# Kernel tuning notes

Measured on AMD Instinct MI355X. Metric: run time of the kernel, lower is better.

## Reference

```python
import jax, jax.numpy as jnp
import numpy as np

N = 8192
D_IN = 512
D_OUT = 64
ALPHA = 0.2  # LeakyReLU negative slope
MASK_VAL = -9e15


def setup_inputs() -> dict:
    key = jax.random.key(0)
    k1, k2, k3, k4 = jax.random.split(key, 4)
    inp = jax.random.normal(k1, (N, D_IN), dtype=jnp.float32)
    adj = (jax.random.uniform(k2, (N, N)) < 0.05).astype(jnp.float32)
    adj = adj.at[jnp.arange(N), jnp.arange(N)].set(1.0)
    W = jax.random.normal(k3, (D_IN, D_OUT), dtype=jnp.float32) * 0.05
    a = jax.random.normal(k4, (2 * D_OUT, 1), dtype=jnp.float32) * 0.05
    return {"input": inp, "adj": adj, "W": W, "a": a}


def reference(input, adj, W, a):
    # h = input @ W : [n, out]
    h = input @ W
    # Algebraic equivalent of the dense pairwise concat:
    # e_ij = leakyrelu([h_i || h_j] . a) = leakyrelu(h_i.a1 + h_j.a2)
    a1, a2 = a[:D_OUT, 0], a[D_OUT:, 0]          # [out], [out]
    e = jax.nn.leaky_relu(
        (h @ a1)[:, None] + (h @ a2)[None, :],    # [n, n]
        negative_slope=ALPHA,
    )
    attention = jnp.where(adj > 0, e, MASK_VAL)
    attention = jax.nn.softmax(attention, axis=1)
    out = attention @ h                            # [n, out]
    return jax.nn.elu(out)                         # end=False branch
```

## Files before the change

### kernel.cpp

```cpp
#include <hip/hip_runtime.h>
#include <hip/hip_bf16.h>

#define N 8192
#define D_IN 512
#define D_OUT 64
#define ALPHA 0.2f
#define BM 16
#define BK 128
#define NSTEP (N / BK)

typedef __attribute__((ext_vector_type(4))) float f32x4;
typedef __attribute__((ext_vector_type(8))) short bf16x8;

static __device__ __forceinline__ unsigned pk_bf16(float lo, float hi) {
    unsigned ulo = __bfloat16_as_ushort(__float2bfloat16(lo));
    unsigned uhi = __bfloat16_as_ushort(__float2bfloat16(hi));
    return (uhi << 16) | ulo;
}

#define BARRIER() do { \
    asm volatile("s_waitcnt lgkmcnt(0)" ::: "memory"); \
    __builtin_amdgcn_sched_barrier(0); \
    __builtin_amdgcn_s_barrier(); \
    __builtin_amdgcn_sched_barrier(0); \
} while (0)

__global__ __launch_bounds__(256) void gat_h_kernel(
    const float* __restrict__ input, const float* __restrict__ W,
    const float* __restrict__ a, unsigned short* __restrict__ hbT,
    float* __restrict__ s1, float* __restrict__ s2)
{
    int wave = (blockIdx.x * 256 + threadIdx.x) >> 6;
    int lane = threadIdx.x & 63;
    int row0 = wave * 8;
    const float* in0 = input + (size_t)row0 * D_IN;
    float a1 = a[lane], a2 = a[D_OUT + lane];
    float acc[8];
#pragma unroll
    for (int r = 0; r < 8; ++r) acc[r] = 0.f;
#pragma unroll 4
    for (int k = 0; k < D_IN; ++k) {
        float wk = W[k * D_OUT + lane];
#pragma unroll
        for (int r = 0; r < 8; ++r)
            acc[r] = fmaf(in0[(size_t)r * D_IN + k], wk, acc[r]);
    }
    uint4 hv;
    hv.x = pk_bf16(acc[0], acc[1]);
    hv.y = pk_bf16(acc[2], acc[3]);
    hv.z = pk_bf16(acc[4], acc[5]);
    hv.w = pk_bf16(acc[6], acc[7]);
    *(uint4*)(hbT + (size_t)lane * N + row0) = hv;
#pragma unroll
    for (int r = 0; r < 8; ++r) {
        float p1 = acc[r] * a1;
        float p2 = acc[r] * a2;
#pragma unroll
        for (int off = 32; off; off >>= 1) {
            p1 += __shfl_xor(p1, off, 64);
            p2 += __shfl_xor(p2, off, 64);
        }
        if (lane == 0) { s1[row0 + r] = p1; s2[row0 + r] = p2; }
    }
}

struct Pref { float4 a0, a1; uint4 h0, h1, h2, h3; };

static __device__ __forceinline__ void issue(Pref& p, const float* ab,
                                             const unsigned short* hb, int j0) {
    p.a0 = *(const float4*)(ab + j0);
    p.a1 = *(const float4*)(ab + j0 + 4);
    p.h0 = *(const uint4*)(hb + j0);
    p.h1 = *(const uint4*)(hb + j0 + 8);
    p.h2 = *(const uint4*)(hb + j0 + 16);
    p.h3 = *(const uint4*)(hb + j0 + 24);
}

__global__ __launch_bounds__(256, 2) void gat_flash_kernel(
    const float* __restrict__ adj, const unsigned short* __restrict__ hbT,
    const float* __restrict__ s1, const float* __restrict__ s2,
    float* __restrict__ out)
{
    __shared__ float s2l[N];
    __shared__ __align__(16) unsigned char Pl[2][BM * BK * 2];
    __shared__ __align__(16) unsigned char Hl[2][D_OUT * BK * 2];
    __shared__ float lsl[BM];

    const int tid  = threadIdx.x;
    const int lane = tid & 63;
    const int wv   = tid >> 6;
    const int r    = tid >> 4;
    const int s    = tid & 15;
    const int hd   = tid >> 2;
    const int hc   = tid & 3;
    const int rg   = blockIdx.x * BM + r;

    {
        const float4* src = (const float4*)s2;
        float4* dst = (float4*)s2l;
        for (int i = tid; i < N / 4; i += 256) dst[i] = src[i];
    }
    const float* adj_base = adj + (size_t)rg * N + s * 8;
    const unsigned short* hb_base = hbT + (size_t)hd * N + hc * 32;
    float s1r = s1[rg];
    float eref;
    float lsum = 0.f;
    f32x4 acc = {0.f, 0.f, 0.f, 0.f};

    auto stage = [&](const Pref& p, int j0, int b) {
        float4 s2a = *(const float4*)(s2l + j0 + s * 8);
        float4 s2b = *(const float4*)(s2l + j0 + s * 8 + 4);
        const float* av0 = (const float*)&p.a0;
        const float* av1 = (const float*)&p.a1;
        const float* sv0 = (const float*)&s2a;
        const float* sv1 = (const float*)&s2b;
        float w[8];
#pragma unroll
        for (int z = 0; z < 4; ++z) {
            float e0 = s1r + sv0[z]; e0 = e0 > 0.f ? e0 : ALPHA * e0;
            float e1 = s1r + sv1[z]; e1 = e1 > 0.f ? e1 : ALPHA * e1;
            float w0 = __expf(e0 - eref);
            float w1 = __expf(e1 - eref);
            w[z]     = av0[z] > 0.f ? w0 : 0.f;
            w[z + 4] = av1[z] > 0.f ? w1 : 0.f;
        }
#pragma unroll
        for (int z = 0; z < 8; ++z) lsum += w[z];
        uint4 pk;
        pk.x = pk_bf16(w[0], w[1]); pk.y = pk_bf16(w[2], w[3]);
        pk.z = pk_bf16(w[4], w[5]); pk.w = pk_bf16(w[6], w[7]);
        *(uint4*)(&Pl[b][r * 256 + ((s * 16) ^ ((r & 7) << 4))]) = pk;
        *(uint4*)(&Hl[b][hd * 256 + ((hc * 64 +  0) ^ ((hd & 7) << 4))]) = p.h0;
        *(uint4*)(&Hl[b][hd * 256 + ((hc * 64 + 16) ^ ((hd & 7) << 4))]) = p.h1;
        *(uint4*)(&Hl[b][hd * 256 + ((hc * 64 + 32) ^ ((hd & 7) << 4))]) = p.h2;
        *(uint4*)(&Hl[b][hd * 256 + ((hc * 64 + 48) ^ ((hd & 7) << 4))]) = p.h3;
    };

    auto mfma_step = [&](int c) {
        const unsigned char* Pc = Pl[c];
        const unsigned char* Hc = Hl[c];
        const int i  = lane & 15;
        const int kb = lane >> 4;
        const int dd = wv * 16 + (lane & 15);
#pragma unroll
        for (int kk = 0; kk < 4; ++kk) {
            uint4 ua = *(const uint4*)(Pc + i * 256 + ((kk * 64 + kb * 16) ^ ((i & 7) << 4)));
            uint4 ub = *(const uint4*)(Hc + dd * 256 + ((kk * 64 + kb * 16) ^ ((dd & 7) << 4)));
            acc = __builtin_amdgcn_mfma_f32_16x16x32_bf16(
                __builtin_bit_cast(bf16x8, ua), __builtin_bit_cast(bf16x8, ub), acc, 0, 0, 0);
        }
    };

    Pref RA, RB;
    issue(RA, adj_base, hb_base, 0);
    issue(RB, adj_base, hb_base, BK);
    __syncthreads();
    {
        float ed = s1r + s2l[rg];
        eref = ed > 0.f ? ed : ALPHA * ed;
    }
    stage(RA, 0, 0);
    issue(RA, adj_base, hb_base, 2 * BK);
    BARRIER();

    for (int ks = 0; ks < NSTEP; ks += 2) {
        mfma_step(0);
        stage(RB, (ks + 1) * BK, 1);
        if (ks + 3 < NSTEP) issue(RB, adj_base, hb_base, (ks + 3) * BK);
        BARRIER();
        mfma_step(1);
        if (ks + 2 < NSTEP) {
            stage(RA, (ks + 2) * BK, 0);
            if (ks + 4 < NSTEP) issue(RA, adj_base, hb_base, (ks + 4) * BK);
        }
        BARRIER();
    }

#pragma unroll
    for (int off = 8; off; off >>= 1) lsum += __shfl_xor(lsum, off, 64);
    if ((tid & 15) == 0) lsl[r] = lsum;
    __syncthreads();

    const int dd = wv * 16 + (lane & 15);
#pragma unroll
    for (int reg = 0; reg < 4; ++reg) {
        int i = (lane >> 4) * 4 + reg;
        float o = acc[reg] / lsl[i];
        o = o > 0.f ? o : expm1f(o);
        out[(size_t)(blockIdx.x * BM + i) * 64 + dd] = o;
    }
}

extern "C" void kernel_launch(void* const* d_in, const int* in_sizes, int n_in,
                              void* d_out, int out_size, void* d_ws, size_t ws_size,
                              hipStream_t stream) {
    const float* input = (const float*)d_in[0];
    const float* adj   = (const float*)d_in[1];
    const float* W     = (const float*)d_in[2];
    const float* a     = (const float*)d_in[3];
    float* out = (float*)d_out;

    unsigned short* hbT = (unsigned short*)d_ws;
    float* s1 = (float*)(hbT + (size_t)N * D_OUT);
    float* s2 = s1 + N;

    gat_h_kernel<<<256, 256, 0, stream>>>(input, W, a, hbT, s1, s2);
    gat_flash_kernel<<<N / BM, 256, 0, stream>>>(adj, hbT, s1, s2, out);
}
```

Measured before the change: 123.5 us.

## Drop LDS s2 staging, prefetch s2 from global, raise occupancy

The flash kernel no longer copies the whole 32 KB s2 vector into shared memory at block start. Each thread now prefetches its s2 slice from global memory (L2-resident) together with adj and h, which frees LDS so three blocks can fit per CU instead of two. The projection kernel also gives each wave 4 rows instead of 8 and doubles the grid, for more parallelism in the small GEMM. The cost is extra global loads and more registers per prefetch buffer, which may pressure the tighter launch bound.

```diff
diff --git a/kernel.cpp b/kernel.cpp
--- a/kernel.cpp
+++ b/kernel.cpp
@@ -32,27 +32,25 @@
 {
     int wave = (blockIdx.x * 256 + threadIdx.x) >> 6;
     int lane = threadIdx.x & 63;
-    int row0 = wave * 8;
+    int row0 = wave * 4;
     const float* in0 = input + (size_t)row0 * D_IN;
     float a1 = a[lane], a2 = a[D_OUT + lane];
-    float acc[8];
+    float acc[4];
 #pragma unroll
-    for (int r = 0; r < 8; ++r) acc[r] = 0.f;
+    for (int r = 0; r < 4; ++r) acc[r] = 0.f;
 #pragma unroll 4
     for (int k = 0; k < D_IN; ++k) {
         float wk = W[k * D_OUT + lane];
 #pragma unroll
-        for (int r = 0; r < 8; ++r)
+        for (int r = 0; r < 4; ++r)
             acc[r] = fmaf(in0[(size_t)r * D_IN + k], wk, acc[r]);
     }
-    uint4 hv;
+    uint2 hv;
     hv.x = pk_bf16(acc[0], acc[1]);
     hv.y = pk_bf16(acc[2], acc[3]);
-    hv.z = pk_bf16(acc[4], acc[5]);
-    hv.w = pk_bf16(acc[6], acc[7]);
-    *(uint4*)(hbT + (size_t)lane * N + row0) = hv;
+    *(uint2*)(hbT + (size_t)lane * N + row0) = hv;
 #pragma unroll
-    for (int r = 0; r < 8; ++r) {
+    for (int r = 0; r < 4; ++r) {
         float p1 = acc[r] * a1;
         float p2 = acc[r] * a2;
 #pragma unroll
@@ -64,24 +62,26 @@
     }
 }
 
-struct Pref { float4 a0, a1; uint4 h0, h1, h2, h3; };
+struct Pref { float4 a0, a1, s0, s1; uint4 h0, h1, h2, h3; };
 
 static __device__ __forceinline__ void issue(Pref& p, const float* ab,
+                                             const float* sb,
                                              const unsigned short* hb, int j0) {
     p.a0 = *(const float4*)(ab + j0);
     p.a1 = *(const float4*)(ab + j0 + 4);
+    p.s0 = *(const float4*)(sb + j0);
+    p.s1 = *(const float4*)(sb + j0 + 4);
     p.h0 = *(const uint4*)(hb + j0);
     p.h1 = *(const uint4*)(hb + j0 + 8);
     p.h2 = *(const uint4*)(hb + j0 + 16);
     p.h3 = *(const uint4*)(hb + j0 + 24);
 }
 
-__global__ __launch_bounds__(256, 2) void gat_flash_kernel(
+__global__ __launch_bounds__(256, 3) void gat_flash_kernel(
     const float* __restrict__ adj, const unsigned short* __restrict__ hbT,
     const float* __restrict__ s1, const float* __restrict__ s2,
     float* __restrict__ out)
 {
-    __shared__ float s2l[N];
     __shared__ __align__(16) unsigned char Pl[2][BM * BK * 2];
     __shared__ __align__(16) unsigned char Hl[2][D_OUT * BK * 2];
     __shared__ float lsl[BM];
@@ -95,25 +95,20 @@
     const int hc   = tid & 3;
     const int rg   = blockIdx.x * BM + r;
 
-    {
-        const float4* src = (const float4*)s2;
-        float4* dst = (float4*)s2l;
-        for (int i = tid; i < N / 4; i += 256) dst[i] = src[i];
-    }
     const float* adj_base = adj + (size_t)rg * N + s * 8;
+    const float* s2_base  = s2 + s * 8;
     const unsigned short* hb_base = hbT + (size_t)hd * N + hc * 32;
     float s1r = s1[rg];
-    float eref;
+    float eref = s1r + s2[rg];
+    eref = eref > 0.f ? eref : ALPHA * eref;
     float lsum = 0.f;
     f32x4 acc = {0.f, 0.f, 0.f, 0.f};
 
-    auto stage = [&](const Pref& p, int j0, int b) {
-        float4 s2a = *(const float4*)(s2l + j0 + s * 8);
-        float4 s2b = *(const float4*)(s2l + j0 + s * 8 + 4);
+    auto stage = [&](const Pref& p, int b) {
         const float* av0 = (const float*)&p.a0;
         const float* av1 = (const float*)&p.a1;
-        const float* sv0 = (const float*)&s2a;
-        const float* sv1 = (const float*)&s2b;
+        const float* sv0 = (const float*)&p.s0;
+        const float* sv1 = (const float*)&p.s1;
         float w[8];
 #pragma unroll
         for (int z = 0; z < 4; ++z) {
@@ -152,26 +147,21 @@
     };
 
     Pref RA, RB;
-    issue(RA, adj_base, hb_base, 0);
-    issue(RB, adj_base, hb_base, BK);
-    __syncthreads();
-    {
-        float ed = s1r + s2l[rg];
-        eref = ed > 0.f ? ed : ALPHA * ed;
-    }
-    stage(RA, 0, 0);
-    issue(RA, adj_base, hb_base, 2 * BK);
+    issue(RA, adj_base, s2_base, hb_base, 0);
+    issue(RB, adj_base, s2_base, hb_base, BK);
+    stage(RA, 0);
+    issue(RA, adj_base, s2_base, hb_base, 2 * BK);
     BARRIER();
 
     for (int ks = 0; ks < NSTEP; ks += 2) {
         mfma_step(0);
-        stage(RB, (ks + 1) * BK, 1);
-        if (ks + 3 < NSTEP) issue(RB, adj_base, hb_base, (ks + 3) * BK);
+        stage(RB, 1);
+        if (ks + 3 < NSTEP) issue(RB, adj_base, s2_base, hb_base, (ks + 3) * BK);
         BARRIER();
         mfma_step(1);
         if (ks + 2 < NSTEP) {
-            stage(RA, (ks + 2) * BK, 0);
-            if (ks + 4 < NSTEP) issue(RA, adj_base, hb_base, (ks + 4) * BK);
+            stage(RA, 0);
+            if (ks + 4 < NSTEP) issue(RA, adj_base, s2_base, hb_base, (ks + 4) * BK);
         }
         BARRIER();
     }
@@ -204,6 +194,6 @@
     float* s1 = (float*)(hbT + (size_t)N * D_OUT);
     float* s2 = s1 + N;
 
-    gat_h_kernel<<<256, 256, 0, stream>>>(input, W, a, hbT, s1, s2);
+    gat_h_kernel<<<512, 256, 0, stream>>>(input, W, a, hbT, s1, s2);
     gat_flash_kernel<<<N / BM, 256, 0, stream>>>(adj, hbT, s1, s2, out);
 }
```

Result: faster. 120.0 us (-2.9%).
